# Optimization experiments

Hardware: AMD Instinct MI355X
Metric: run time of the kernel (lower is better)

Reference implementation:

```python
import jax, jax.numpy as jnp
import numpy as np

N = 100000      # nodes
E = 1600000     # edges
D_IN = 64       # input feature dim
H = 64          # hidden dim
HNUM = 128      # number of direct virtual nodes (blocks)
NCONV = 2       # layers-1 conv layers in module_list
NMLP = 2        # layers-1 virtual-node MLPs (all applied each conv iter)
NEG_SLOPE = 0.2


def setup_inputs() -> dict:
    key = jax.random.key(0)
    ks = jax.random.split(key, 16)
    s = 0.1
    inp = {
        "x": jax.random.normal(ks[0], (N, D_IN), jnp.float32),
        "edge_index": jax.random.randint(ks[1], (2, E), 0, N, dtype=jnp.int32),
        "h_blocks": jax.random.randint(ks[2], (N,), 0, HNUM, dtype=jnp.int32),
        "h_levels": jax.random.randint(ks[3], (N,), 0, 4, dtype=jnp.int32),
        "h_num": HNUM,
        # initial GATConv(input->hidden): lin weight (no bias), att_src, att_dst, out bias
        "W0": jax.random.normal(ks[4], (D_IN, H), jnp.float32) * s,
        "a_src0": jax.random.normal(ks[5], (H,), jnp.float32) * s,
        "a_dst0": jax.random.normal(ks[6], (H,), jnp.float32) * s,
        "b0": jnp.zeros((H,), jnp.float32),
        # stacked module_list GATConv(hidden->hidden) params
        "Wl": jax.random.normal(ks[7], (NCONV, H, H), jnp.float32) * s,
        "a_srcl": jax.random.normal(ks[8], (NCONV, H), jnp.float32) * s,
        "a_dstl": jax.random.normal(ks[9], (NCONV, H), jnp.float32) * s,
        "bl": jnp.zeros((NCONV, H), jnp.float32),
        # virtual node embedding, torch init constant 0
        "vn_emb": jnp.zeros((1, H), jnp.float32),
        # virtual-node MLPs: Linear->ReLU->Linear->ReLU, weights stored (in,out)
        "mlp_W1": jax.random.normal(ks[10], (NMLP, H, H), jnp.float32) * s,
        "mlp_b1": jnp.zeros((NMLP, H), jnp.float32),
        "mlp_W2": jax.random.normal(ks[11], (NMLP, H, H), jnp.float32) * s,
        "mlp_b2": jnp.zeros((NMLP, H), jnp.float32),
    }
    return inp


def gat_conv(x, src, dst, W, a_src, a_dst, b, n_nodes):
    """PyG GATConv, heads=1, concat, add_self_loops=True, negative_slope=0.2."""
    h = x @ W                                    # [N, H]
    loop = jnp.arange(n_nodes, dtype=src.dtype)
    s = jnp.concatenate([src, loop])             # [E+N]
    d = jnp.concatenate([dst, loop])
    a_s = h @ a_src                              # [N]
    a_d = h @ a_dst
    e = jax.nn.leaky_relu(a_s[s] + a_d[d], negative_slope=NEG_SLOPE)  # [E+N]
    # segment softmax over destination nodes (self loops cover every segment)
    m = jax.ops.segment_max(e, d, num_segments=n_nodes)
    w = jnp.exp(e - m[d])
    denom = jax.ops.segment_sum(w, d, num_segments=n_nodes)
    alpha = w / (denom[d] + 1e-16)               # [E+N]
    out = jax.ops.segment_sum(h[s] * alpha[:, None], d, num_segments=n_nodes)
    return out + b


def reference(x, edge_index, h_blocks, h_levels, h_num,
              W0, a_src0, a_dst0, b0, Wl, a_srcl, a_dstl, bl,
              vn_emb, mlp_W1, mlp_b1, mlp_W2, mlp_b2):
    src, dst = edge_index[0], edge_index[1]
    n_nodes = x.shape[0]
    out = gat_conv(x, src, dst, W0, a_src0, a_dst0, b0, n_nodes)
    # embedding lookup of all-zero indices == broadcast of row 0
    vn_direct = jnp.broadcast_to(vn_emb[0], (h_num, vn_emb.shape[1]))  # [HNUM, H]
    vn_root = vn_emb                                                   # [1, H]
    for l in range(NCONV):
        out = out + vn_direct[h_blocks]
        out = gat_conv(out, src, dst, Wl[l], a_srcl[l], a_dstl[l], bl[l], n_nodes)
        vn_direct = jax.ops.segment_sum(out, h_blocks, num_segments=h_num) + vn_direct
        vn_direct = vn_direct + vn_root
        vn_root = jnp.sum(vn_direct, axis=0, keepdims=True) + vn_root
        # NB: the original applies EVERY vn-MLP inside each conv iteration
        for j in range(NMLP):
            vn_direct = jax.nn.relu(jax.nn.relu(vn_direct @ mlp_W1[j] + mlp_b1[j]) @ mlp_W2[j] + mlp_b2[j])
            vn_root = jax.nn.relu(jax.nn.relu(vn_root @ mlp_W1[j] + mlp_b1[j]) @ mlp_W2[j] + mlp_b2[j])
    return out
```

## Files before the change

### kernel.cpp

```cpp
#include <hip/hip_runtime.h>
#include <hip/hip_fp16.h>
#include <math.h>

#define HD 64
#define HNUM 128
#define NMLP 2
#define BSH 8
#define MAXNB 512
#define EPB 4096

typedef unsigned int uint_t;
typedef unsigned short ushort_t;
typedef _Float16 h8 __attribute__((ext_vector_type(8)));
typedef float vf4 __attribute__((ext_vector_type(4)));

union H8U { h8 v; uint_t u[4]; };
union H4  { uint2 u; _Float16 h[4]; };

__device__ __forceinline__ float lrelu(float x){ return fmaxf(x, 0.2f*x); }

__device__ __forceinline__ uint_t pk2(float a, float b){
    return (uint_t)__half_as_ushort(__float2half_rn(a)) |
           ((uint_t)__half_as_ushort(__float2half_rn(b)) << 16);
}

__global__ __launch_bounds__(256) void k_bcnt(const int* __restrict__ dst, int* __restrict__ gb,
                                              int E, int NB){
    __shared__ int h[MAXNB];
    int t = threadIdx.x;
    for(int i=t;i<NB;i+=256) h[i] = 0;
    __syncthreads();
    for(int e = blockIdx.x*256 + t; e < E; e += gridDim.x*256)
        atomicAdd(&h[dst[e]>>BSH], 1);
    __syncthreads();
    for(int i=t;i<NB;i+=256) if(h[i]) atomicAdd(&gb[i], h[i]);
}

__global__ __launch_bounds__(512) void k_bscan(const int* __restrict__ gb, int* __restrict__ bbase,
                                               int* __restrict__ gcur, int NB){
    __shared__ int s[512];
    int t = threadIdx.x;
    int v = (t < NB) ? gb[t] : 0;
    s[t] = v; __syncthreads();
    for(int o=1;o<512;o<<=1){
        int u = (t >= o) ? s[t-o] : 0;
        __syncthreads();
        s[t] += u;
        __syncthreads();
    }
    if(t < NB){ int ex = s[t] - v; bbase[t] = ex; gcur[t] = ex; }
}

__global__ __launch_bounds__(256) void k_bin(const int* __restrict__ src, const int* __restrict__ dst,
                                             int* __restrict__ gcur, uint_t* __restrict__ bdata,
                                             int E, int NB){
    __shared__ int cnt[MAXNB];
    __shared__ int base[MAXNB];
    int t = threadIdx.x;
    for(int i=t;i<NB;i+=256) cnt[i] = 0;
    __syncthreads();
    int s0 = blockIdx.x*EPB;
    uint_t pk[16]; int bk[16], off[16];
    #pragma unroll
    for(int i=0;i<16;i++){
        int e = s0 + i*256 + t;
        if(e < E){
            int sv = src[e], dv = dst[e];
            pk[i]  = ((uint_t)sv << 8) | (uint_t)(dv & 255);
            bk[i]  = dv >> BSH;
            off[i] = atomicAdd(&cnt[bk[i]], 1);
        }
    }
    __syncthreads();
    for(int i=t;i<NB;i+=256) base[i] = cnt[i] ? atomicAdd(&gcur[i], cnt[i]) : 0;
    __syncthreads();
    #pragma unroll
    for(int i=0;i<16;i++){
        int e = s0 + i*256 + t;
        if(e < E) bdata[base[bk[i]] + off[i]] = pk[i];
    }
}

__global__ __launch_bounds__(256) void k_bfuse(const uint_t* __restrict__ bdata, const int* __restrict__ bbase,
                                               const int* __restrict__ gb, int* __restrict__ rp,
                                               int* __restrict__ col, int n, int NB, int E){
    __shared__ int h[256];
    __shared__ int sc[256];
    int b = blockIdx.x, t = threadIdx.x;
    int beg = bbase[b], cnt = gb[b];
    h[t] = 0; __syncthreads();
    for(int i=t;i<cnt;i+=256) atomicAdd(&h[bdata[beg+i] & 255], 1);
    __syncthreads();
    int v = h[t];
    sc[t] = v; __syncthreads();
    for(int o=1;o<256;o<<=1){
        int u = (t >= o) ? sc[t-o] : 0;
        __syncthreads();
        sc[t] += u;
        __syncthreads();
    }
    int excl = sc[t] - v;
    int node = (b<<BSH) + t;
    if(node < n) rp[node] = beg + excl;
    if(b == NB-1 && t == 255) rp[n] = E;
    __syncthreads();
    sc[t] = excl;
    __syncthreads();
    for(int i=t;i<cnt;i+=256){
        uint_t e = bdata[beg+i];
        int pos = atomicAdd(&sc[e & 255], 1);
        col[beg + pos] = (int)(e >> 8);
    }
}

__global__ __launch_bounds__(256) void k_vcnt(const int* __restrict__ hb, int* __restrict__ vcnt, int n){
    __shared__ int h[HNUM];
    int t = threadIdx.x;
    if(t < HNUM) h[t] = 0;
    __syncthreads();
    for(int i = blockIdx.x*256 + t; i < n; i += gridDim.x*256) atomicAdd(&h[hb[i]], 1);
    __syncthreads();
    if(t < HNUM && h[t]) atomicAdd(&vcnt[t], h[t]);
}

__global__ __launch_bounds__(128) void k_vscan(const int* __restrict__ vcnt, int* __restrict__ vrp,
                                               int* __restrict__ vcur, int n){
    __shared__ int s[HNUM];
    int t = threadIdx.x;
    int v = vcnt[t];
    s[t] = v; __syncthreads();
    for(int o=1;o<HNUM;o<<=1){
        int u = (t >= o) ? s[t-o] : 0;
        __syncthreads();
        s[t] += u;
        __syncthreads();
    }
    int ex = s[t] - v;
    vrp[t] = ex; vcur[t] = ex;
    if(t == HNUM-1) vrp[HNUM] = n;
}

__global__ __launch_bounds__(256) void k_vbin(const int* __restrict__ hb, int* __restrict__ vcur,
                                              int* __restrict__ perm, int n){
    __shared__ int cnt[HNUM];
    __shared__ int base[HNUM];
    int t = threadIdx.x;
    if(t < HNUM) cnt[t] = 0;
    __syncthreads();
    int s0 = blockIdx.x*2048;
    int hv[8], off[8];
    #pragma unroll
    for(int i=0;i<8;i++){
        int nd = s0 + i*256 + t;
        if(nd < n){ hv[i] = hb[nd]; off[i] = atomicAdd(&cnt[hv[i]], 1); }
    }
    __syncthreads();
    if(t < HNUM) base[t] = cnt[t] ? atomicAdd(&vcur[t], cnt[t]) : 0;
    __syncthreads();
    #pragma unroll
    for(int i=0;i<8;i++){
        int nd = s0 + i*256 + t;
        if(nd < n) perm[base[hv[i]] + off[i]] = nd;
    }
}

__global__ __launch_bounds__(256) void k_wcvt(
    const float* __restrict__ W0, const float* __restrict__ as0, const float* __restrict__ ad0,
    const float* __restrict__ Wl, const float* __restrict__ asl, const float* __restrict__ adl,
    uint4* __restrict__ Wf3, float* __restrict__ waf3)
{
    __shared__ float wa[2][64];
    int L = blockIdx.x, t = threadIdx.x;
    const float* W  = (L==0) ? W0  : Wl  + (L-1)*HD*HD;
    const float* as = (L==0) ? as0 : asl + (L-1)*HD;
    const float* ad = (L==0) ? ad0 : adl + (L-1)*HD;
    if(t < 128){
        int sd = t>>6, k = t&63;
        const float* av = sd ? ad : as;
        float acc = 0.f;
        for(int c=0;c<HD;c++) acc = fmaf(W[k*HD+c], av[c], acc);
        wa[sd][k] = acc;
    }
    __syncthreads();
    for(int it = t; it < 512; it += 256){
        int lane = it&63, s = (it>>6)&1, tile = it>>7;
        int g = lane>>4, m = lane&15, c = tile*16 + m;
        ushort_t h[8];
        #pragma unroll
        for(int i=0;i<8;i++){
            int k = s*32 + g*4 + (i&3) + 16*(i>>2);
            h[i] = __half_as_ushort(__float2half_rn(W[k*HD + c]));
        }
        uint4 q;
        q.x = (uint_t)h[0] | ((uint_t)h[1]<<16);
        q.y = (uint_t)h[2] | ((uint_t)h[3]<<16);
        q.z = (uint_t)h[4] | ((uint_t)h[5]<<16);
        q.w = (uint_t)h[6] | ((uint_t)h[7]<<16);
        Wf3[(size_t)L*512 + (tile*2+s)*64 + lane] = q;
    }
    if(t < 128){
        int lane = t&63, sd = t>>6, g = lane>>4;
        #pragma unroll
        for(int j4=0;j4<4;j4++){
            float v[4];
            #pragma unroll
            for(int e=0;e<4;e++){
                int j = j4*4 + e;
                int k = (j>>3)*32 + g*4 + (j&3) + 16*((j>>2)&1);
                v[e] = wa[sd][k];
            }
            float* dstp = waf3 + ((size_t)L*8 + sd*4 + j4)*64*4 + lane*4;
            dstp[0]=v[0]; dstp[1]=v[1]; dstp[2]=v[2]; dstp[3]=v[3];
        }
    }
}

__global__ __launch_bounds__(256) void k_gemm(
    const float* __restrict__ IN, const float* __restrict__ addrow,
    const float* __restrict__ addtab, const int* __restrict__ hb,
    const uint4* __restrict__ Wf, const float* __restrict__ waf,
    uint_t* __restrict__ Hw, float* __restrict__ AS, float* __restrict__ AD,
    int n)
{
    __shared__ ushort_t sx[4][1024];
    int t = threadIdx.x, lane = t&63, wv = t>>6;
    int g = lane>>4, m = lane&15;
    ushort_t* sb = sx[wv];

    H8U B[8];
    #pragma unroll
    for(int f=0; f<8; f++){
        uint4 q = Wf[f*64 + lane];
        B[f].u[0]=q.x; B[f].u[1]=q.y; B[f].u[2]=q.z; B[f].u[3]=q.w;
    }
    vf4 wS[4], wD[4];
    #pragma unroll
    for(int j4=0;j4<4;j4++){
        const float* ps = waf + ((size_t)0*4 + j4)*256 + lane*4;
        const float* pd = waf + ((size_t)1*4 + j4)*256 + lane*4;
        wS[j4] = vf4{ps[0],ps[1],ps[2],ps[3]};
        wD[j4] = vf4{pd[0],pd[1],pd[2],pd[3]};
    }
    float ar0=0,ar1=0,ar2=0,ar3=0;
    if(addrow){
        const float* a = &addrow[m*4];
        ar0=a[0]; ar1=a[1]; ar2=a[2]; ar3=a[3];
    }

    int ntiles = (n + 15) >> 4;
    int wgid = (blockIdx.x*256 + t) >> 6;
    int nw = gridDim.x*4;
    for(int tile = wgid; tile < ntiles; tile += nw){
        int rb = tile*16;
        #pragma unroll
        for(int p=0;p<4;p++){
            int row = p*4 + g;
            int rowc = min(rb + row, n-1);
            float4 x4 = *(const float4*)&IN[(size_t)rowc*HD + m*4];
            if(addrow){ x4.x+=ar0; x4.y+=ar1; x4.z+=ar2; x4.w+=ar3; }
            if(addtab){
                int b = hb[rowc];
                float4 a4 = *(const float4*)&addtab[b*HD + m*4];
                x4.x+=a4.x; x4.y+=a4.y; x4.z+=a4.z; x4.w+=a4.w;
            }
            uint2 pq; pq.x = pk2(x4.x, x4.y); pq.y = pk2(x4.z, x4.w);
            int idx = (row*64 + m*4) ^ ((row&7)<<3);
            *(uint2*)&sb[idx] = pq;
        }
        int xr = (m&7)<<3;
        H8U A0, A1;
        {
            uint2 c0 = *(uint2*)&sb[(m*64 +  0 + g*4) ^ xr];
            uint2 c1 = *(uint2*)&sb[(m*64 + 16 + g*4) ^ xr];
            A0.u[0]=c0.x; A0.u[1]=c0.y; A0.u[2]=c1.x; A0.u[3]=c1.y;
            uint2 c2 = *(uint2*)&sb[(m*64 + 32 + g*4) ^ xr];
            uint2 c3 = *(uint2*)&sb[(m*64 + 48 + g*4) ^ xr];
            A1.u[0]=c2.x; A1.u[1]=c2.y; A1.u[2]=c3.x; A1.u[3]=c3.y;
        }
        float t1 = 0.f, t2 = 0.f;
        #pragma unroll
        for(int i=0;i<8;i++){
            float xv = (float)A0.v[i];
            t1 = fmaf(xv, wS[i>>2][i&3], t1);
            t2 = fmaf(xv, wD[i>>2][i&3], t2);
        }
        #pragma unroll
        for(int i=0;i<8;i++){
            float xv = (float)A1.v[i];
            t1 = fmaf(xv, wS[2+(i>>2)][i&3], t1);
            t2 = fmaf(xv, wD[2+(i>>2)][i&3], t2);
        }
        t1 += __shfl_xor(t1, 16, 64); t1 += __shfl_xor(t1, 32, 64);
        t2 += __shfl_xor(t2, 16, 64); t2 += __shfl_xor(t2, 32, 64);
        if(lane < 16 && rb + lane < n){ AS[rb+lane] = t1; AD[rb+lane] = t2; }
        vf4 z = {0.f,0.f,0.f,0.f};
        vf4 a0 = __builtin_amdgcn_mfma_f32_16x16x32_f16(A0.v, B[0].v, z, 0,0,0);
        a0     = __builtin_amdgcn_mfma_f32_16x16x32_f16(A1.v, B[1].v, a0, 0,0,0);
        vf4 a1 = __builtin_amdgcn_mfma_f32_16x16x32_f16(A0.v, B[2].v, z, 0,0,0);
        a1     = __builtin_amdgcn_mfma_f32_16x16x32_f16(A1.v, B[3].v, a1, 0,0,0);
        vf4 a2 = __builtin_amdgcn_mfma_f32_16x16x32_f16(A0.v, B[4].v, z, 0,0,0);
        a2     = __builtin_amdgcn_mfma_f32_16x16x32_f16(A1.v, B[5].v, a2, 0,0,0);
        vf4 a3 = __builtin_amdgcn_mfma_f32_16x16x32_f16(A0.v, B[6].v, z, 0,0,0);
        a3     = __builtin_amdgcn_mfma_f32_16x16x32_f16(A1.v, B[7].v, a3, 0,0,0);
        #pragma unroll
        for(int rr=0;rr<4;rr++){
            int row = rb + g*4 + rr;
            if(row < n){
                Hw[(size_t)row*32 + m]      = pk2(a0[rr], a1[rr]);
                Hw[(size_t)row*32 + 16 + m] = pk2(a2[rr], a3[rr]);
            }
        }
    }
}

__global__ __launch_bounds__(256) void k_agg(
    const uint_t* __restrict__ Hb, const float* __restrict__ AS, const float* __restrict__ AD,
    const int* __restrict__ rp, const int* __restrict__ col,
    const float* __restrict__ bias, float* __restrict__ OUT, int n)
{
    int t = threadIdx.x, lane = t & 63;
    int p = lane & 15;
    int qb = lane & 48;
    int w0 = 2*p;
    int c00 = 32*(w0>>4)+(w0&15), c01 = c00+16;
    int c10 = c00+1, c11 = c00+17;
    float b00 = bias[c00], b01 = bias[c01], b10 = bias[c10], b11 = bias[c11];
    int wv  = (blockIdx.x*256 + t) >> 6;
    int nwv = gridDim.x*4;
    for(int base = wv*4; base < n; base += nwv*4){
        int dq = min(base + (qb>>4), n-1);
        float ad = AD[dq];
        float wself = __expf(lrelu(AS[dq] + ad));
        H4 hd; hd.u = *(const uint2*)&Hb[(size_t)dq*32 + w0];
        float4 acc;
        acc.x = (float)hd.h[0]*wself; acc.y = (float)hd.h[1]*wself;
        acc.z = (float)hd.h[2]*wself; acc.w = (float)hd.h[3]*wself;
        float sacc = 0.f;
        int beg = rp[dq], end = rp[dq+1];
        int cnt = end - beg;
        int nit = (cnt + 15) >> 4;
        nit = max(nit, __shfl_xor(nit, 16, 64));
        nit = max(nit, __shfl_xor(nit, 32, 64));
        for(int it = 0; it < nit; it++){
            int j = beg + it*16 + p;
            bool valid = j < end;
            int sj = dq;
            if(cnt > 0) sj = col[valid ? j : end - 1];
            float wj = 0.f;
            if(valid) wj = __expf(lrelu(AS[sj] + ad));
            sacc += wj;
            int ccnt = cnt - it*16;
            ccnt = ccnt < 0 ? 0 : (ccnt > 16 ? 16 : ccnt);
            int emax = ccnt;
            emax = max(emax, __shfl_xor(emax, 16, 64));
            emax = max(emax, __shfl_xor(emax, 32, 64));
            int e = 0;
            for(; e + 4 <= emax; e += 4){
                float wq0 = __shfl(wj, qb+e,   64);
                float wq1 = __shfl(wj, qb+e+1, 64);
                float wq2 = __shfl(wj, qb+e+2, 64);
                float wq3 = __shfl(wj, qb+e+3, 64);
                int   sq0 = __shfl(sj, qb+e,   64);
                int   sq1 = __shfl(sj, qb+e+1, 64);
                int   sq2 = __shfl(sj, qb+e+2, 64);
                int   sq3 = __shfl(sj, qb+e+3, 64);
                H4 v0; v0.u = *(const uint2*)&Hb[(size_t)sq0*32 + w0];
                H4 v1; v1.u = *(const uint2*)&Hb[(size_t)sq1*32 + w0];
                H4 v2; v2.u = *(const uint2*)&Hb[(size_t)sq2*32 + w0];
                H4 v3; v3.u = *(const uint2*)&Hb[(size_t)sq3*32 + w0];
                acc.x = fmaf(wq0, (float)v0.h[0], acc.x);
                acc.y = fmaf(wq0, (float)v0.h[1], acc.y);
                acc.z = fmaf(wq0, (float)v0.h[2], acc.z);
                acc.w = fmaf(wq0, (float)v0.h[3], acc.w);
                acc.x = fmaf(wq1, (float)v1.h[0], acc.x);
                acc.y = fmaf(wq1, (float)v1.h[1], acc.y);
                acc.z = fmaf(wq1, (float)v1.h[2], acc.z);
                acc.w = fmaf(wq1, (float)v1.h[3], acc.w);
                acc.x = fmaf(wq2, (float)v2.h[0], acc.x);
                acc.y = fmaf(wq2, (float)v2.h[1], acc.y);
                acc.z = fmaf(wq2, (float)v2.h[2], acc.z);
                acc.w = fmaf(wq2, (float)v2.h[3], acc.w);
                acc.x = fmaf(wq3, (float)v3.h[0], acc.x);
                acc.y = fmaf(wq3, (float)v3.h[1], acc.y);
                acc.z = fmaf(wq3, (float)v3.h[2], acc.z);
                acc.w = fmaf(wq3, (float)v3.h[3], acc.w);
            }
            for(; e < emax; e++){
                float wq = __shfl(wj, qb+e, 64);
                int   sq = __shfl(sj, qb+e, 64);
                H4 v; v.u = *(const uint2*)&Hb[(size_t)sq*32 + w0];
                acc.x = fmaf(wq, (float)v.h[0], acc.x);
                acc.y = fmaf(wq, (float)v.h[1], acc.y);
                acc.z = fmaf(wq, (float)v.h[2], acc.z);
                acc.w = fmaf(wq, (float)v.h[3], acc.w);
            }
        }
        sacc += __shfl_xor(sacc, 1, 64);
        sacc += __shfl_xor(sacc, 2, 64);
        sacc += __shfl_xor(sacc, 4, 64);
        sacc += __shfl_xor(sacc, 8, 64);
        float s = wself + sacc;
        float inv = 1.f/(s + 1e-16f);
        if(base + (qb>>4) < n){
            OUT[(size_t)dq*HD + c00] = fmaf(acc.x, inv, b00);
            OUT[(size_t)dq*HD + c01] = fmaf(acc.y, inv, b01);
            OUT[(size_t)dq*HD + c10] = fmaf(acc.z, inv, b10);
            OUT[(size_t)dq*HD + c11] = fmaf(acc.w, inv, b11);
        }
    }
}

__global__ __launch_bounds__(256) void k_vsum(const float* __restrict__ OUT, const int* __restrict__ perm,
                                              const int* __restrict__ vrp, float* __restrict__ vnS){
    int t = threadIdx.x, lane = t & 63, w = t >> 6;
    int g = blockIdx.x >> 3, sub = blockIdx.x & 7;
    int wig = sub*4 + w;
    int beg = vrp[g], end = vrp[g+1];
    float a0=0.f, a1=0.f, a2=0.f, a3=0.f;
    int i = beg + wig;
    for(; i + 96 < end; i += 128){
        int p0 = perm[i], p1 = perm[i+32], p2 = perm[i+64], p3 = perm[i+96];
        a0 += OUT[(size_t)p0*HD + lane];
        a1 += OUT[(size_t)p1*HD + lane];
        a2 += OUT[(size_t)p2*HD + lane];
        a3 += OUT[(size_t)p3*HD + lane];
    }
    for(; i < end; i += 32) a0 += OUT[(size_t)perm[i]*HD + lane];
    float a = (a0+a1)+(a2+a3);
    unsafeAtomicAdd(&vnS[g*HD + lane], a);
}

__global__ __launch_bounds__(64) void k_vn(
    const float* __restrict__ vnS, const float* __restrict__ vne,
    const float* __restrict__ W1, const float* __restrict__ B1,
    const float* __restrict__ W2, const float* __restrict__ B2,
    float* __restrict__ vnD)
{
    __shared__ float sx[HD];
    int lane = threadIdx.x;
    int r = blockIdx.x;
    float ve = vne[lane];
    float a = vnS[r*HD + lane] + ve + ve;
    for(int j=0;j<NMLP;j++){
        const float* w1 = W1 + j*HD*HD; const float* b1 = B1 + j*HD;
        const float* w2 = W2 + j*HD*HD; const float* b2 = B2 + j*HD;
        __syncthreads();
        sx[lane] = a;
        __syncthreads();
        float t = b1[lane];
        #pragma unroll
        for(int in=0;in<HD;in++) t = fmaf(sx[in], w1[in*HD + lane], t);
        t = fmaxf(t, 0.f);
        __syncthreads();
        sx[lane] = t;
        __syncthreads();
        float u = b2[lane];
        #pragma unroll
        for(int in=0;in<HD;in++) u = fmaf(sx[in], w2[in*HD + lane], u);
        a = fmaxf(u, 0.f);
    }
    vnD[r*HD + lane] = a;
}

extern "C" void kernel_launch(void* const* d_in, const int* in_sizes, int n_in,
                              void* d_out, int out_size, void* d_ws, size_t ws_size,
                              hipStream_t stream)
{
    const float* x   = (const float*)d_in[0];
    const int*   ei  = (const int*)d_in[1];
    const int*   hb  = (const int*)d_in[2];
    const float* W0  = (const float*)d_in[5];
    const float* as0 = (const float*)d_in[6];
    const float* ad0 = (const float*)d_in[7];
    const float* b0  = (const float*)d_in[8];
    const float* Wl  = (const float*)d_in[9];
    const float* asl = (const float*)d_in[10];
    const float* adl = (const float*)d_in[11];
    const float* bl  = (const float*)d_in[12];
    const float* vne = (const float*)d_in[13];
    const float* mW1 = (const float*)d_in[14];
    const float* mb1 = (const float*)d_in[15];
    const float* mW2 = (const float*)d_in[16];
    const float* mb2 = (const float*)d_in[17];

    int N = in_sizes[0]/HD;
    int E = in_sizes[1]/2;
    const int* src = ei;
    const int* dst = ei + E;
    int NB = (N + (1<<BSH) - 1) >> BSH;

    char* p = (char*)d_ws;
    float* f_h   = (float*)p; p += (size_t)N*HD*4;
    float* f_as  = (float*)p; p += (size_t)N*4;
    float* f_ad  = (float*)p; p += (size_t)N*4;
    float* f_vnD = (float*)p; p += HNUM*HD*4;
    float* f_vnS = (float*)p; p += HNUM*HD*4;
    int*   i_vcnt= (int*)p;   p += HNUM*4;
    int*   i_vrp = (int*)p;   p += (HNUM+1)*4;
    int*   i_vcur= (int*)p;   p += HNUM*4;
    int*   i_perm= (int*)p;   p += (size_t)N*4;
    int*   i_rp  = (int*)p;   p += (size_t)(N+1)*4;
    int*   i_gb  = (int*)p;   p += MAXNB*4;
    int*   i_bb  = (int*)p;   p += MAXNB*4;
    int*   i_gc  = (int*)p;   p += MAXNB*4;
    int*   i_col = (int*)p;   p += (size_t)E*4;
    uint4* Wf3   = (uint4*)p; p += 3*512*16;
    float* waf3  = (float*)p; p += 3*8*64*4*4;
    uint_t* bdata= (uint_t*)f_h;
    uint_t* Hw   = (uint_t*)f_h;

    float* outb = (float*)d_out;

    k_wcvt<<<3, 256, 0, stream>>>(W0, as0, ad0, Wl, asl, adl, Wf3, waf3);

    hipMemsetAsync(i_gb, 0, MAXNB*4, stream);
    hipMemsetAsync(f_vnS, 0, HNUM*HD*4 + HNUM*4, stream);
    k_bcnt <<<512, 256, 0, stream>>>(dst, i_gb, E, NB);
    k_bscan<<<1, 512, 0, stream>>>(i_gb, i_bb, i_gc, NB);
    k_bin  <<<(E+EPB-1)/EPB, 256, 0, stream>>>(src, dst, i_gc, bdata, E, NB);
    k_bfuse<<<NB, 256, 0, stream>>>(bdata, i_bb, i_gb, i_rp, i_col, N, NB, E);
    k_vcnt <<<128, 256, 0, stream>>>(hb, i_vcnt, N);
    k_vscan<<<1, 128, 0, stream>>>(i_vcnt, i_vrp, i_vcur, N);
    k_vbin <<<(N+2047)/2048, 256, 0, stream>>>(hb, i_vcur, i_perm, N);

    int ga = 4096;
    int gg = 768;
    k_gemm<<<gg, 256, 0, stream>>>(x, nullptr, nullptr, hb, Wf3, waf3, Hw, f_as, f_ad, N);
    k_agg <<<ga, 256, 0, stream>>>(Hw, f_as, f_ad, i_rp, i_col, b0, outb, N);
    k_gemm<<<gg, 256, 0, stream>>>(outb, vne, nullptr, hb, Wf3 + 512, waf3 + 2048, Hw, f_as, f_ad, N);
    k_agg <<<ga, 256, 0, stream>>>(Hw, f_as, f_ad, i_rp, i_col, bl, outb, N);
    k_vsum<<<HNUM*8, 256, 0, stream>>>(outb, i_perm, i_vrp, f_vnS);
    k_vn  <<<HNUM, 64, 0, stream>>>(f_vnS, vne, mW1, mb1, mW2, mb2, f_vnD);
    k_gemm<<<gg, 256, 0, stream>>>(outb, nullptr, f_vnD, hb, Wf3 + 1024, waf3 + 4096, Hw, f_as, f_ad, N);
    k_agg <<<ga, 256, 0, stream>>>(Hw, f_as, f_ad, i_rp, i_col, bl + HD, outb, N);
}
```

Before: 244.1 us.

## Precompute per-edge attention weights in separate kernel before aggregation

Adds a per-edge kernel that computes exp(leaky_relu(AS[src]+AD[dst])) for every CSR edge into a buffer, using a new dst array written during CSR build. The aggregation kernel then reads those weights and column indices directly per lane, with no cross-lane shuffles and no exp on the gather path. The cost is an extra kernel launch per layer and additional reads and writes of about 2×E ints/floats, plus redundant per-lane loads of the same weights and columns across the 16 lanes of each node.

```diff
diff --git a/kernel.cpp b/kernel.cpp
--- a/kernel.cpp
+++ b/kernel.cpp
@@ -83,7 +83,8 @@
 
 __global__ __launch_bounds__(256) void k_bfuse(const uint_t* __restrict__ bdata, const int* __restrict__ bbase,
                                                const int* __restrict__ gb, int* __restrict__ rp,
-                                               int* __restrict__ col, int n, int NB, int E){
+                                               int* __restrict__ col, int* __restrict__ dstarr,
+                                               int n, int NB, int E){
     __shared__ int h[256];
     __shared__ int sc[256];
     int b = blockIdx.x, t = threadIdx.x;
@@ -108,8 +109,21 @@
     __syncthreads();
     for(int i=t;i<cnt;i+=256){
         uint_t e = bdata[beg+i];
-        int pos = atomicAdd(&sc[e & 255], 1);
-        col[beg + pos] = (int)(e >> 8);
+        int lid = e & 255;
+        int pos = atomicAdd(&sc[lid], 1);
+        col[beg + pos]    = (int)(e >> 8);
+        dstarr[beg + pos] = (b<<BSH) + lid;
+    }
+}
+
+__global__ __launch_bounds__(256) void k_ew(const int* __restrict__ col, const int* __restrict__ dstarr,
+                                            const float* __restrict__ AS, const float* __restrict__ AD,
+                                            float* __restrict__ wbuf, int E){
+    int b0 = blockIdx.x*1024 + threadIdx.x;
+    #pragma unroll
+    for(int k=0;k<4;k++){
+        int e = b0 + k*256;
+        if(e < E) wbuf[e] = __expf(lrelu(AS[col[e]] + AD[dstarr[e]]));
     }
 }
 
@@ -315,90 +329,67 @@
 
 __global__ __launch_bounds__(256) void k_agg(
     const uint_t* __restrict__ Hb, const float* __restrict__ AS, const float* __restrict__ AD,
-    const int* __restrict__ rp, const int* __restrict__ col,
+    const int* __restrict__ rp, const int* __restrict__ col, const float* __restrict__ wbuf,
     const float* __restrict__ bias, float* __restrict__ OUT, int n)
 {
     int t = threadIdx.x, lane = t & 63;
     int p = lane & 15;
     int qb = lane & 48;
-    int w0 = 2*p;
-    int c00 = 32*(w0>>4)+(w0&15), c01 = c00+16;
+    int wd = 2*p;
+    int c00 = 32*(wd>>4)+(wd&15), c01 = c00+16;
     int c10 = c00+1, c11 = c00+17;
     float b00 = bias[c00], b01 = bias[c01], b10 = bias[c10], b11 = bias[c11];
     int wv  = (blockIdx.x*256 + t) >> 6;
     int nwv = gridDim.x*4;
     for(int base = wv*4; base < n; base += nwv*4){
         int dq = min(base + (qb>>4), n-1);
-        float ad = AD[dq];
-        float wself = __expf(lrelu(AS[dq] + ad));
-        H4 hd; hd.u = *(const uint2*)&Hb[(size_t)dq*32 + w0];
+        float wself = __expf(lrelu(AS[dq] + AD[dq]));
+        H4 hd; hd.u = *(const uint2*)&Hb[(size_t)dq*32 + wd];
         float4 acc;
         acc.x = (float)hd.h[0]*wself; acc.y = (float)hd.h[1]*wself;
         acc.z = (float)hd.h[2]*wself; acc.w = (float)hd.h[3]*wself;
         float sacc = 0.f;
         int beg = rp[dq], end = rp[dq+1];
         int cnt = end - beg;
-        int nit = (cnt + 15) >> 4;
-        nit = max(nit, __shfl_xor(nit, 16, 64));
-        nit = max(nit, __shfl_xor(nit, 32, 64));
-        for(int it = 0; it < nit; it++){
-            int j = beg + it*16 + p;
-            bool valid = j < end;
-            int sj = dq;
-            if(cnt > 0) sj = col[valid ? j : end - 1];
-            float wj = 0.f;
-            if(valid) wj = __expf(lrelu(AS[sj] + ad));
-            sacc += wj;
-            int ccnt = cnt - it*16;
-            ccnt = ccnt < 0 ? 0 : (ccnt > 16 ? 16 : ccnt);
-            int emax = ccnt;
-            emax = max(emax, __shfl_xor(emax, 16, 64));
-            emax = max(emax, __shfl_xor(emax, 32, 64));
-            int e = 0;
-            for(; e + 4 <= emax; e += 4){
-                float wq0 = __shfl(wj, qb+e,   64);
-                float wq1 = __shfl(wj, qb+e+1, 64);
-                float wq2 = __shfl(wj, qb+e+2, 64);
-                float wq3 = __shfl(wj, qb+e+3, 64);
-                int   sq0 = __shfl(sj, qb+e,   64);
-                int   sq1 = __shfl(sj, qb+e+1, 64);
-                int   sq2 = __shfl(sj, qb+e+2, 64);
-                int   sq3 = __shfl(sj, qb+e+3, 64);
-                H4 v0; v0.u = *(const uint2*)&Hb[(size_t)sq0*32 + w0];
-                H4 v1; v1.u = *(const uint2*)&Hb[(size_t)sq1*32 + w0];
-                H4 v2; v2.u = *(const uint2*)&Hb[(size_t)sq2*32 + w0];
-                H4 v3; v3.u = *(const uint2*)&Hb[(size_t)sq3*32 + w0];
-                acc.x = fmaf(wq0, (float)v0.h[0], acc.x);
-                acc.y = fmaf(wq0, (float)v0.h[1], acc.y);
-                acc.z = fmaf(wq0, (float)v0.h[2], acc.z);
-                acc.w = fmaf(wq0, (float)v0.h[3], acc.w);
-                acc.x = fmaf(wq1, (float)v1.h[0], acc.x);
-                acc.y = fmaf(wq1, (float)v1.h[1], acc.y);
-                acc.z = fmaf(wq1, (float)v1.h[2], acc.z);
-                acc.w = fmaf(wq1, (float)v1.h[3], acc.w);
-                acc.x = fmaf(wq2, (float)v2.h[0], acc.x);
-                acc.y = fmaf(wq2, (float)v2.h[1], acc.y);
-                acc.z = fmaf(wq2, (float)v2.h[2], acc.z);
-                acc.w = fmaf(wq2, (float)v2.h[3], acc.w);
-                acc.x = fmaf(wq3, (float)v3.h[0], acc.x);
-                acc.y = fmaf(wq3, (float)v3.h[1], acc.y);
-                acc.z = fmaf(wq3, (float)v3.h[2], acc.z);
-                acc.w = fmaf(wq3, (float)v3.h[3], acc.w);
-            }
-            for(; e < emax; e++){
-                float wq = __shfl(wj, qb+e, 64);
-                int   sq = __shfl(sj, qb+e, 64);
-                H4 v; v.u = *(const uint2*)&Hb[(size_t)sq*32 + w0];
-                acc.x = fmaf(wq, (float)v.h[0], acc.x);
-                acc.y = fmaf(wq, (float)v.h[1], acc.y);
-                acc.z = fmaf(wq, (float)v.h[2], acc.z);
-                acc.w = fmaf(wq, (float)v.h[3], acc.w);
-            }
-        }
-        sacc += __shfl_xor(sacc, 1, 64);
-        sacc += __shfl_xor(sacc, 2, 64);
-        sacc += __shfl_xor(sacc, 4, 64);
-        sacc += __shfl_xor(sacc, 8, 64);
+        int cmax = cnt;
+        cmax = max(cmax, __shfl_xor(cmax, 16, 64));
+        cmax = max(cmax, __shfl_xor(cmax, 32, 64));
+        for(int e0 = 0; e0 < cmax; e0 += 4){
+            bool v0 = e0   < cnt, v1 = e0+1 < cnt, v2 = e0+2 < cnt, v3 = e0+3 < cnt;
+            int j0 = v0 ? beg+e0   : 0;
+            int j1 = v1 ? beg+e0+1 : 0;
+            int j2 = v2 ? beg+e0+2 : 0;
+            int j3 = v3 ? beg+e0+3 : 0;
+            float w0 = v0 ? wbuf[j0] : 0.f;
+            float w1 = v1 ? wbuf[j1] : 0.f;
+            float w2 = v2 ? wbuf[j2] : 0.f;
+            float w3 = v3 ? wbuf[j3] : 0.f;
+            int s0 = v0 ? col[j0] : dq;
+            int s1 = v1 ? col[j1] : dq;
+            int s2 = v2 ? col[j2] : dq;
+            int s3 = v3 ? col[j3] : dq;
+            sacc += (w0+w1)+(w2+w3);
+            H4 h0; h0.u = *(const uint2*)&Hb[(size_t)s0*32 + wd];
+            H4 h1; h1.u = *(const uint2*)&Hb[(size_t)s1*32 + wd];
+            H4 h2; h2.u = *(const uint2*)&Hb[(size_t)s2*32 + wd];
+            H4 h3; h3.u = *(const uint2*)&Hb[(size_t)s3*32 + wd];
+            acc.x = fmaf(w0, (float)h0.h[0], acc.x);
+            acc.y = fmaf(w0, (float)h0.h[1], acc.y);
+            acc.z = fmaf(w0, (float)h0.h[2], acc.z);
+            acc.w = fmaf(w0, (float)h0.h[3], acc.w);
+            acc.x = fmaf(w1, (float)h1.h[0], acc.x);
+            acc.y = fmaf(w1, (float)h1.h[1], acc.y);
+            acc.z = fmaf(w1, (float)h1.h[2], acc.z);
+            acc.w = fmaf(w1, (float)h1.h[3], acc.w);
+            acc.x = fmaf(w2, (float)h2.h[0], acc.x);
+            acc.y = fmaf(w2, (float)h2.h[1], acc.y);
+            acc.z = fmaf(w2, (float)h2.h[2], acc.z);
+            acc.w = fmaf(w2, (float)h2.h[3], acc.w);
+            acc.x = fmaf(w3, (float)h3.h[0], acc.x);
+            acc.y = fmaf(w3, (float)h3.h[1], acc.y);
+            acc.z = fmaf(w3, (float)h3.h[2], acc.z);
+            acc.w = fmaf(w3, (float)h3.h[3], acc.w);
+        }
         float s = wself + sacc;
         float inv = 1.f/(s + 1e-16f);
         if(base + (qb>>4) < n){
@@ -504,6 +495,8 @@
     int*   i_bb  = (int*)p;   p += MAXNB*4;
     int*   i_gc  = (int*)p;   p += MAXNB*4;
     int*   i_col = (int*)p;   p += (size_t)E*4;
+    int*   i_dst = (int*)p;   p += (size_t)E*4;
+    float* f_w   = (float*)p; p += (size_t)E*4;
     uint4* Wf3   = (uint4*)p; p += 3*512*16;
     float* waf3  = (float*)p; p += 3*8*64*4*4;
     uint_t* bdata= (uint_t*)f_h;
@@ -518,19 +511,23 @@
     k_bcnt <<<512, 256, 0, stream>>>(dst, i_gb, E, NB);
     k_bscan<<<1, 512, 0, stream>>>(i_gb, i_bb, i_gc, NB);
     k_bin  <<<(E+EPB-1)/EPB, 256, 0, stream>>>(src, dst, i_gc, bdata, E, NB);
-    k_bfuse<<<NB, 256, 0, stream>>>(bdata, i_bb, i_gb, i_rp, i_col, N, NB, E);
+    k_bfuse<<<NB, 256, 0, stream>>>(bdata, i_bb, i_gb, i_rp, i_col, i_dst, N, NB, E);
     k_vcnt <<<128, 256, 0, stream>>>(hb, i_vcnt, N);
     k_vscan<<<1, 128, 0, stream>>>(i_vcnt, i_vrp, i_vcur, N);
     k_vbin <<<(N+2047)/2048, 256, 0, stream>>>(hb, i_vcur, i_perm, N);
 
     int ga = 4096;
     int gg = 768;
+    int ge = (E + 1023)/1024;
     k_gemm<<<gg, 256, 0, stream>>>(x, nullptr, nullptr, hb, Wf3, waf3, Hw, f_as, f_ad, N);
-    k_agg <<<ga, 256, 0, stream>>>(Hw, f_as, f_ad, i_rp, i_col, b0, outb, N);
+    k_ew  <<<ge, 256, 0, stream>>>(i_col, i_dst, f_as, f_ad, f_w, E);
+    k_agg <<<ga, 256, 0, stream>>>(Hw, f_as, f_ad, i_rp, i_col, f_w, b0, outb, N);
     k_gemm<<<gg, 256, 0, stream>>>(outb, vne, nullptr, hb, Wf3 + 512, waf3 + 2048, Hw, f_as, f_ad, N);
-    k_agg <<<ga, 256, 0, stream>>>(Hw, f_as, f_ad, i_rp, i_col, bl, outb, N);
+    k_ew  <<<ge, 256, 0, stream>>>(i_col, i_dst, f_as, f_ad, f_w, E);
+    k_agg <<<ga, 256, 0, stream>>>(Hw, f_as, f_ad, i_rp, i_col, f_w, bl, outb, N);
     k_vsum<<<HNUM*8, 256, 0, stream>>>(outb, i_perm, i_vrp, f_vnS);
     k_vn  <<<HNUM, 64, 0, stream>>>(f_vnS, vne, mW1, mb1, mW2, mb2, f_vnD);
     k_gemm<<<gg, 256, 0, stream>>>(outb, nullptr, f_vnD, hb, Wf3 + 1024, waf3 + 4096, Hw, f_as, f_ad, N);
-    k_agg <<<ga, 256, 0, stream>>>(Hw, f_as, f_ad, i_rp, i_col, bl + HD, outb, N);
-}
+    k_ew  <<<ge, 256, 0, stream>>>(i_col, i_dst, f_as, f_ad, f_w, E);
+    k_agg <<<ga, 256, 0, stream>>>(Hw, f_as, f_ad, i_rp, i_col, f_w, bl + HD, outb, N);
+}
```

After: 286.8 us. +17.5%, slower.
